# Optimization experiments

Hardware: AMD Instinct MI355X
Metric: run time of the kernel (lower is better)

## Reference

```python
import jax, jax.numpy as jnp
import numpy as np

B = 8192
E = 8
H = 128
NUM_CLASSES = 3
SIM_THRESHOLD = 0.8
EFF_THRESHOLD = 0.1
TARGET_TEMP = 1.0
W_LB, W_EFF, W_CONS, W_ENT, W_TEMP = 0.1, 0.05, 0.1, 0.01, 0.01


def setup_inputs() -> dict:
    key = jax.random.key(0)
    k1, k2, k3, k4 = jax.random.split(key, 4)
    logits = jax.random.normal(k1, (B, NUM_CLASSES), dtype=jnp.float32)
    targets = jax.random.randint(k2, (B,), 0, NUM_CLASSES, dtype=jnp.int64)
    raw = jax.random.uniform(k3, (B, E), dtype=jnp.float32)
    routing_probs = raw / raw.sum(axis=-1, keepdims=True)  # rows sum to 1
    input_embeddings = jax.random.uniform(k4, (B, H), dtype=jnp.float32)
    temperature = jnp.ones((1,), dtype=jnp.float32)
    return {
        "logits": logits,
        "targets": targets,
        "routing_probs": routing_probs,
        "input_embeddings": input_embeddings,
        "temperature": temperature,
    }


def _dynamo_loss(logits, routing_probs, input_embeddings, temperature, targets):
    # --- task loss: cross entropy (sentiment) ---
    logp_cls = jax.nn.log_softmax(logits, axis=-1)
    task_loss = -jnp.take_along_axis(logp_cls, targets[:, None], axis=-1).mean()

    # --- load balance: var(mean usage) / (1/E)^2 (torch.var unbiased) ---
    expert_usage = routing_probs.mean(axis=0)  # [E]
    lb_loss = W_LB * jnp.var(expert_usage, ddof=1) * (E ** 2)

    # --- efficiency: sum of probs below threshold, averaged over batch ---
    small = jnp.where(routing_probs < EFF_THRESHOLD, routing_probs, 0.0)
    eff_loss = W_EFF * small.sum(axis=-1).mean()

    # --- consistency: masked pairwise KL over similar samples ---
    nrm = input_embeddings / jnp.linalg.norm(input_embeddings, axis=-1, keepdims=True)
    sim = nrm @ nrm.T  # [B, B]
    mask = (sim > SIM_THRESHOLD) & ~jnp.eye(B, dtype=bool)
    logp = jax.nn.log_softmax(routing_probs, axis=-1)  # [B, E]
    p = jnp.exp(logp)
    a = jnp.sum(p * logp, axis=-1)  # [B], sum_e p_j log p_j
    # KL(i,j) = sum_e p_j (log p_j - log p_i) = a[j] - logp[i] . p[j]
    kl = a[None, :] - logp @ p.T  # [B, B]
    num_pairs = mask.sum()
    kl_sum = jnp.sum(jnp.where(mask, kl, 0.0))
    cons_loss = W_CONS * jnp.where(num_pairs > 0, kl_sum / jnp.maximum(num_pairs, 1), 0.0)

    # --- entropy regularization (maximize entropy of routing_probs-as-probs) ---
    eps = 1e-8
    entropy = -jnp.sum(routing_probs * jnp.log(routing_probs + eps), axis=-1)
    ent_loss = W_ENT * (-entropy.mean())

    # --- temperature regularization ---
    temp_loss = W_TEMP * jnp.mean((temperature - TARGET_TEMP) ** 2)

    return task_loss + lb_loss + eff_loss + cons_loss + ent_loss + temp_loss


def reference(logits, targets, routing_probs, input_embeddings, temperature):
    return _dynamo_loss(logits, routing_probs, input_embeddings, temperature, targets)
```

## Files before the change

### kernel.cpp

```cpp
#include <hip/hip_runtime.h>
#include <stdint.h>

#define B_SZ 8192
#define LOG8 2.0794415416798357f
#define NTILE 2080

typedef __attribute__((ext_vector_type(8))) short short8;
typedef __attribute__((ext_vector_type(4))) float floatx4;

__device__ inline unsigned short f2bf(float f) {
    unsigned int u = __float_as_uint(f);
    u = (u + 0x7FFFu + ((u >> 16) & 1u)) >> 16;
    return (unsigned short)u;
}
__device__ inline float bf2f(unsigned short s) {
    return __uint_as_float(((unsigned int)s) << 16);
}
__device__ inline float wredf(float x) {
#pragma unroll
    for (int o = 32; o; o >>= 1) x += __shfl_down(x, o);
    return x;
}
__device__ inline int wredi(int x) {
#pragma unroll
    for (int o = 32; o; o >>= 1) x += __shfl_down(x, o);
    return x;
}


__global__ __launch_bounds__(512) void prep_all(
    const float* __restrict__ logits,
    const int* __restrict__ targets,
    const float* __restrict__ routing,
    const float* __restrict__ emb,
    unsigned short* __restrict__ nrm,
    unsigned short* __restrict__ nlq,
    unsigned short* __restrict__ pb,
    float* __restrict__ aprime,
    float* __restrict__ prepslot) {
    __shared__ float pred[8][11];
    const int bid = blockIdx.x;
    const int lane = threadIdx.x & 63;
    const int wave = threadIdx.x >> 6;

    if (bid < 256) {
#pragma unroll
        for (int iter = 0; iter < 4; ++iter) {
            int row = (((iter << 8) + bid) << 3) + wave;
            const float2* e2 = (const float2*)(emb + (size_t)row * 128);
            float2 v = e2[lane];
            float ss = v.x * v.x + v.y * v.y;
            ss = wredf(ss);
            ss = __shfl(ss, 0);
            float inv = rsqrtf(ss);
            ushort2 o;
            o.x = f2bf(v.x * inv);
            o.y = f2bf(v.y * inv);
            ((ushort2*)(nrm + (size_t)row * 128))[lane] = o;
        }
        return;
    }

    int row = ((bid - 256) << 9) + threadIdx.x;

    const float4* r4 = (const float4*)(routing + (size_t)row * 8);
    float4 va = r4[0], vb = r4[1];
    float v[8] = {va.x, va.y, va.z, va.w, vb.x, vb.y, vb.z, vb.w};

    float mx = v[0];
#pragma unroll
    for (int e = 1; e < 8; ++e) mx = fmaxf(mx, v[e]);
    float ex[8], s = 0.f;
#pragma unroll
    for (int e = 0; e < 8; ++e) { ex[e] = expf(v[e] - mx); s += ex[e]; }
    float ls = logf(s);
    float inv_s = 1.f / s;

    union { unsigned short u[8]; uint4 q; } lu, pu;
    float ap = 0.f;
#pragma unroll
    for (int e = 0; e < 8; ++e) {
        unsigned short pe = f2bf(ex[e] * inv_s);
        unsigned short le = f2bf(v[e] - mx - ls + LOG8);
        pu.u[e] = pe;
        lu.u[e] = le ^ 0x8000;
        ap += bf2f(pe) * bf2f(le);
    }
    ((uint4*)nlq)[row] = lu.q;
    ((uint4*)pb)[row] = pu.q;
    aprime[row] = ap;

    float eff = 0.f, ent = 0.f;
#pragma unroll
    for (int e = 0; e < 8; ++e) {
        if (v[e] < 0.1f) eff += v[e];
        ent += v[e] * logf(v[e] + 1e-8f);
    }

    const float* lg = logits + (size_t)row * 3;
    float a0 = lg[0], a1 = lg[1], a2 = lg[2];
    float mm = fmaxf(a0, fmaxf(a1, a2));
    float lse = mm + logf(expf(a0 - mm) + expf(a1 - mm) + expf(a2 - mm));
    int tg = targets[row];
    float tv = (tg == 0) ? a0 : ((tg == 1) ? a1 : a2);
    float task = lse - tv;

    task = wredf(task);
    eff = wredf(eff);
    ent = wredf(ent);
    float cs[8];
#pragma unroll
    for (int e = 0; e < 8; ++e) cs[e] = wredf(v[e]);

    if (lane == 0) {
        pred[wave][0] = task;
        pred[wave][1] = eff;
        pred[wave][2] = ent;
#pragma unroll
        for (int e = 0; e < 8; ++e) pred[wave][3 + e] = cs[e];
    }
    __syncthreads();
    if (threadIdx.x < 11) {
        float s2 = 0.f;
#pragma unroll
        for (int w = 0; w < 8; ++w) s2 += pred[w][threadIdx.x];
        prepslot[(bid - 256) * 11 + threadIdx.x] = s2;
    }
}

__global__ __launch_bounds__(512, 4) void tile_sym(
    const unsigned short* __restrict__ nrm,
    const unsigned short* __restrict__ nlq,
    const unsigned short* __restrict__ pb,
    const float* __restrict__ aprime,
    float* __restrict__ klslot,
    unsigned int* __restrict__ cntslot) {
    __shared__ uint4 sh[2][128][16];

    const int t = threadIdx.x;
    const int L = blockIdx.x;

    int bi = (int)((129.0f - sqrtf((float)(16641 - 8 * L))) * 0.5f);
    int T = bi * 64 - ((bi * (bi - 1)) >> 1);
    while (L < T) { --bi; T = bi * 64 - ((bi * (bi - 1)) >> 1); }
    while (L >= T + (64 - bi)) { T += 64 - bi; ++bi; }
    const int bj = bi + (L - T);
    const bool diag = (bi == bj);
    const int iBase = bi << 7, jBase = bj << 7;

    const uint4* n4 = (const uint4*)nrm;
#pragma unroll
    for (int it = 0; it < 4; ++it) {
        int c = t + (it << 9);
        int row = c >> 4, g = c & 15;
        int gp = g ^ (row & 15);
        uint4 va = n4[((size_t)(iBase + row) << 4) + g];
        uint4 vb = n4[((size_t)(jBase + row) << 4) + g];
        sh[0][row][gp] = va;
        sh[1][row][gp] = vb;
    }

    const int wave = t >> 6, lane = t & 63;
    const int wr = wave >> 2, wc = wave & 3;
    const int m = lane & 15, q = lane >> 4;
    const short8 zero8 = (short8){0, 0, 0, 0, 0, 0, 0, 0};

    short8 crA[4], crB[2];
#pragma unroll
    for (int a = 0; a < 4; ++a) {
        int ri = iBase + (wr << 6) + (a << 4) + m;
        short8 v = zero8;
        if (q == 0) v = *(const short8*)&nlq[(size_t)ri << 3];
        else if (q == 1) { if (!diag) v = *(const short8*)&pb[(size_t)ri << 3]; }
        else if (q == 2) {
            v[1] = (short)0x3F80;
            if (!diag) v[0] = (short)f2bf(aprime[ri]);
        }
        crA[a] = v;
    }
#pragma unroll
    for (int b = 0; b < 2; ++b) {
        int cj = jBase + (wc << 5) + (b << 4) + m;
        short8 v = zero8;
        if (q == 0) v = *(const short8*)&pb[(size_t)cj << 3];
        else if (q == 1) v = *(const short8*)&nlq[(size_t)cj << 3];
        else if (q == 2) {
            v[0] = (short)0x3F80;
            v[1] = (short)f2bf(aprime[cj]);
        }
        crB[b] = v;
    }

    __syncthreads();

    const unsigned short* Ab = (const unsigned short*)&sh[0][0][0];
    const unsigned short* Bb = (const unsigned short*)&sh[1][0][0];

    floatx4 simacc[4][2];
#pragma unroll
    for (int a = 0; a < 4; ++a)
#pragma unroll
        for (int b = 0; b < 2; ++b) simacc[a][b] = (floatx4){0.f, 0.f, 0.f, 0.f};

#pragma unroll
    for (int ks = 0; ks < 4; ++ks) {
        const int g = (ks << 2) + q;
        short8 af[4], bfr[2];
#pragma unroll
        for (int a = 0; a < 4; ++a) {
            int ra = (wr << 6) + (a << 4) + m;
            af[a] = *(const short8*)&Ab[(ra << 7) + ((g ^ m) << 3)];
        }
#pragma unroll
        for (int b = 0; b < 2; ++b) {
            int rb = (wc << 5) + (b << 4) + m;
            bfr[b] = *(const short8*)&Bb[(rb << 7) + ((g ^ m) << 3)];
        }
#pragma unroll
        for (int a = 0; a < 4; ++a)
#pragma unroll
            for (int b = 0; b < 2; ++b)
                simacc[a][b] = __builtin_amdgcn_mfma_f32_16x16x32_bf16(
                    af[a], bfr[b], simacc[a][b], 0, 0, 0);
    }

    float klLocal = 0.f;
    int cntLocal = 0;
#pragma unroll
    for (int a = 0; a < 4; ++a) {
        const int gRow0 = iBase + (wr << 6) + (a << 4) + (q << 2);
#pragma unroll
        for (int b = 0; b < 2; ++b) {
            const int gCol = jBase + (wc << 5) + (b << 4) + m;
            floatx4 cr = __builtin_amdgcn_mfma_f32_16x16x32_bf16(
                crA[a], crB[b], (floatx4){0.f, 0.f, 0.f, 0.f}, 0, 0, 0);
            if (diag) {
#pragma unroll
                for (int r = 0; r < 4; ++r) {
                    if ((simacc[a][b][r] > 0.8f) && (gRow0 + r != gCol)) {
                        klLocal += cr[r];
                        cntLocal += 1;
                    }
                }
            } else {
#pragma unroll
                for (int r = 0; r < 4; ++r) {
                    if (simacc[a][b][r] > 0.8f) {
                        klLocal += cr[r];
                        cntLocal += 2;
                    }
                }
            }
        }
    }

    klLocal = wredf(klLocal);
    cntLocal = wredi(cntLocal);

    __syncthreads();
    float* redk = (float*)&sh[0][0][0];
    int* redc = (int*)(redk + 8);
    if (lane == 0) { redk[wave] = klLocal; redc[wave] = cntLocal; }
    __syncthreads();

    if (t == 0) {
        float k = 0.f;
        int c = 0;
#pragma unroll
        for (int w = 0; w < 8; ++w) { k += redk[w]; c += redc[w]; }
        klslot[L] = k;
        cntslot[L] = (unsigned int)c;
    }
}

__global__ void finalize_k(const float* __restrict__ klslot,
                           const unsigned int* __restrict__ cntslot,
                           const float* __restrict__ prepslot,
                           const float* __restrict__ temp,
                           float* __restrict__ out) {
    __shared__ float sk[4];
    __shared__ int sc[4];
    __shared__ float sp[11];
    const int t = threadIdx.x, lane = t & 63, wave = t >> 6;

    float k = 0.f;
    int c = 0;
    for (int i = t; i < NTILE; i += 256) { k += klslot[i]; c += (int)cntslot[i]; }
    k = wredf(k);
    c = wredi(c);
    if (lane == 0) { sk[wave] = k; sc[wave] = c; }
    if (t < 11) {
        float s = 0.f;
        for (int r = 0; r < 16; ++r) s += prepslot[r * 11 + t];
        sp[t] = s;
    }
    __syncthreads();
    if (t == 0) {
        float K = sk[0] + sk[1] + sk[2] + sk[3];
        int C = sc[0] + sc[1] + sc[2] + sc[3];
        const float invB = 1.f / (float)B_SZ;
        float task = sp[0] * invB;
        float eff = 0.05f * sp[1] * invB;
        float entl = 0.01f * sp[2] * invB;
        float cons = 0.1f * (C > 0 ? K / (float)C : 0.f);
        float u[8], mean = 0.f;
        for (int e = 0; e < 8; ++e) { u[e] = sp[3 + e] * invB; mean += u[e]; }
        mean *= 0.125f;
        float var = 0.f;
        for (int e = 0; e < 8; ++e) { float d = u[e] - mean; var += d * d; }
        var *= (1.f / 7.f);
        float lb = 0.1f * var * 64.f;
        float tt = temp[0] - 1.f;
        out[0] = task + lb + eff + cons + entl + 0.01f * tt * tt;
    }
}

extern "C" void kernel_launch(void* const* d_in, const int* in_sizes, int n_in,
                              void* d_out, int out_size, void* d_ws, size_t ws_size,
                              hipStream_t stream) {
    const float* logits = (const float*)d_in[0];
    const int* targets = (const int*)d_in[1];
    const float* routing = (const float*)d_in[2];
    const float* emb = (const float*)d_in[3];
    const float* temp = (const float*)d_in[4];

    char* ws = (char*)d_ws;
    unsigned short* nrm = (unsigned short*)ws;
    unsigned short* nlq = (unsigned short*)(ws + 2097152);
    unsigned short* pb = (unsigned short*)(ws + 2228224);
    float* aprime = (float*)(ws + 2359296);
    float* klslot = (float*)(ws + 2392064);
    unsigned int* cntslot = (unsigned int*)(ws + 2400384);
    float* prepslot = (float*)(ws + 2408704);

    prep_all<<<272, 512, 0, stream>>>(logits, targets, routing, emb,
                                      nrm, nlq, pb, aprime, prepslot);
    tile_sym<<<NTILE, 512, 0, stream>>>(nrm, nlq, pb, aprime, klslot, cntslot);
    finalize_k<<<1, 256, 0, stream>>>(klslot, cntslot, prepslot, temp,
                                      (float*)d_out);
}
```

Before: 103.2 us.

## Load embedding tiles via async global_load_lds in two K-halves

Replaces register-staged global-to-LDS copies of the normalized-embedding tiles with direct global_load_lds async copies, split into two K halves. The first half's MFMAs run while the second half is still loading, and the LDS layout changes to a per-half 8-slot XOR swizzle. The aim is to cut VGPR staging and overlap load latency with compute. It relies on correct synchronization of the async LDS writes: __syncthreads may not wait on vmcnt for these loads, which could cause races.

```diff
diff --git a/kernel.cpp b/kernel.cpp
--- a/kernel.cpp
+++ b/kernel.cpp
@@ -7,6 +7,13 @@
 
 typedef __attribute__((ext_vector_type(8))) short short8;
 typedef __attribute__((ext_vector_type(4))) float floatx4;
+
+typedef __attribute__((address_space(1))) const uint4 guint4;
+typedef __attribute__((address_space(3))) uint4 luint4;
+
+__device__ inline void async_cp16(const uint4* g, uint4* l) {
+    __builtin_amdgcn_global_load_lds((guint4*)g, (luint4*)l, 16, 0, 0);
+}
 
 __device__ inline unsigned short f2bf(float f) {
     unsigned int u = __float_as_uint(f);
@@ -135,10 +142,11 @@
     const float* __restrict__ aprime,
     float* __restrict__ klslot,
     unsigned int* __restrict__ cntslot) {
-    __shared__ uint4 sh[2][128][16];
+    __shared__ uint4 sh[4096];
 
     const int t = threadIdx.x;
     const int L = blockIdx.x;
+    const int wave = t >> 6, lane = t & 63;
 
     int bi = (int)((129.0f - sqrtf((float)(16641 - 8 * L))) * 0.5f);
     int T = bi * 64 - ((bi * (bi - 1)) >> 1);
@@ -149,18 +157,22 @@
     const int iBase = bi << 7, jBase = bj << 7;
 
     const uint4* n4 = (const uint4*)nrm;
-#pragma unroll
-    for (int it = 0; it < 4; ++it) {
-        int c = t + (it << 9);
-        int row = c >> 4, g = c & 15;
-        int gp = g ^ (row & 15);
-        uint4 va = n4[((size_t)(iBase + row) << 4) + g];
-        uint4 vb = n4[((size_t)(jBase + row) << 4) + g];
-        sh[0][row][gp] = va;
-        sh[1][row][gp] = vb;
-    }
-
-    const int wave = t >> 6, lane = t & 63;
+    const int s0 = t & 7, r0 = t >> 3;
+    const int s1 = (t + 512) & 7, r1 = (t + 512) >> 3;
+    const int g0 = s0 ^ (r0 & 7), g1 = s1 ^ (r1 & 7);
+
+    async_cp16(&n4[((size_t)(iBase + r0) << 4) + g0], sh + (wave << 6));
+    async_cp16(&n4[((size_t)(iBase + r1) << 4) + g1], sh + 512 + (wave << 6));
+    async_cp16(&n4[((size_t)(jBase + r0) << 4) + g0], sh + 1024 + (wave << 6));
+    async_cp16(&n4[((size_t)(jBase + r1) << 4) + g1], sh + 1536 + (wave << 6));
+
+    __syncthreads();
+
+    async_cp16(&n4[((size_t)(iBase + r0) << 4) + 8 + g0], sh + 2048 + (wave << 6));
+    async_cp16(&n4[((size_t)(iBase + r1) << 4) + 8 + g1], sh + 2560 + (wave << 6));
+    async_cp16(&n4[((size_t)(jBase + r0) << 4) + 8 + g0], sh + 3072 + (wave << 6));
+    async_cp16(&n4[((size_t)(jBase + r1) << 4) + 8 + g1], sh + 3584 + (wave << 6));
+
     const int wr = wave >> 2, wc = wave & 3;
     const int m = lane & 15, q = lane >> 4;
     const short8 zero8 = (short8){0, 0, 0, 0, 0, 0, 0, 0};
@@ -191,31 +203,46 @@
         crB[b] = v;
     }
 
-    __syncthreads();
-
-    const unsigned short* Ab = (const unsigned short*)&sh[0][0][0];
-    const unsigned short* Bb = (const unsigned short*)&sh[1][0][0];
-
     floatx4 simacc[4][2];
 #pragma unroll
     for (int a = 0; a < 4; ++a)
 #pragma unroll
         for (int b = 0; b < 2; ++b) simacc[a][b] = (floatx4){0.f, 0.f, 0.f, 0.f};
 
-#pragma unroll
-    for (int ks = 0; ks < 4; ++ks) {
-        const int g = (ks << 2) + q;
+    const int m7 = m & 7;
+    const int raOff = (wr << 6) << 3;
+    const int rbOff = (wc << 5) << 3;
+
+#pragma unroll
+    for (int ks = 0; ks < 2; ++ks) {
+        const int sg = ((ks << 2) + q) ^ m7;
         short8 af[4], bfr[2];
 #pragma unroll
-        for (int a = 0; a < 4; ++a) {
-            int ra = (wr << 6) + (a << 4) + m;
-            af[a] = *(const short8*)&Ab[(ra << 7) + ((g ^ m) << 3)];
-        }
-#pragma unroll
-        for (int b = 0; b < 2; ++b) {
-            int rb = (wc << 5) + (b << 4) + m;
-            bfr[b] = *(const short8*)&Bb[(rb << 7) + ((g ^ m) << 3)];
-        }
+        for (int a = 0; a < 4; ++a)
+            af[a] = *(const short8*)(sh + raOff + (((a << 4) + m) << 3) + sg);
+#pragma unroll
+        for (int b = 0; b < 2; ++b)
+            bfr[b] = *(const short8*)(sh + 1024 + rbOff + (((b << 4) + m) << 3) + sg);
+#pragma unroll
+        for (int a = 0; a < 4; ++a)
+#pragma unroll
+            for (int b = 0; b < 2; ++b)
+                simacc[a][b] = __builtin_amdgcn_mfma_f32_16x16x32_bf16(
+                    af[a], bfr[b], simacc[a][b], 0, 0, 0);
+    }
+
+    __syncthreads();
+
+#pragma unroll
+    for (int ks = 0; ks < 2; ++ks) {
+        const int sg = ((ks << 2) + q) ^ m7;
+        short8 af[4], bfr[2];
+#pragma unroll
+        for (int a = 0; a < 4; ++a)
+            af[a] = *(const short8*)(sh + 2048 + raOff + (((a << 4) + m) << 3) + sg);
+#pragma unroll
+        for (int b = 0; b < 2; ++b)
+            bfr[b] = *(const short8*)(sh + 3072 + rbOff + (((b << 4) + m) << 3) + sg);
 #pragma unroll
         for (int a = 0; a < 4; ++a)
 #pragma unroll
@@ -258,7 +285,7 @@
     cntLocal = wredi(cntLocal);
 
     __syncthreads();
-    float* redk = (float*)&sh[0][0][0];
+    float* redk = (float*)sh;
     int* redc = (int*)(redk + 8);
     if (lane == 0) { redk[wave] = klLocal; redc[wave] = cntLocal; }
     __syncthreads();
```

Measured after the change: 101.9 us. No clear change (-1.2%).

## Stage A tile via async global-to-LDS loads and read B fragments directly

Applied to the files above, without the earlier changes.

The A-side embedding tile is now copied into shared memory with the hardware's direct global-to-LDS load path instead of going through registers. The B-side fragments are loaded straight from global memory into registers, which halves LDS usage and drops the B-side LDS reads. The similarity MFMA loop now runs before the routing fragment setup. This is meant to cut register staging and LDS traffic and to allow more concurrent blocks, at the cost of uncoalesced-ish direct global fragment loads and reliance on the async LDS copy's layout semantics (the wave-based LDS destination must match the swizzled read indexing).

```diff
diff --git a/kernel.cpp b/kernel.cpp
--- a/kernel.cpp
+++ b/kernel.cpp
@@ -7,6 +7,13 @@
 
 typedef __attribute__((ext_vector_type(8))) short short8;
 typedef __attribute__((ext_vector_type(4))) float floatx4;
+
+typedef __attribute__((address_space(1))) const uint4 guint4;
+typedef __attribute__((address_space(3))) uint4 luint4;
+
+__device__ inline void async_cp16(const uint4* g, uint4* l) {
+    __builtin_amdgcn_global_load_lds((guint4*)g, (luint4*)l, 16, 0, 0);
+}
 
 __device__ inline unsigned short f2bf(float f) {
     unsigned int u = __float_as_uint(f);
@@ -135,10 +142,11 @@
     const float* __restrict__ aprime,
     float* __restrict__ klslot,
     unsigned int* __restrict__ cntslot) {
-    __shared__ uint4 sh[2][128][16];
+    __shared__ uint4 sh[2048];
 
     const int t = threadIdx.x;
     const int L = blockIdx.x;
+    const int wave = t >> 6, lane = t & 63;
 
     int bi = (int)((129.0f - sqrtf((float)(16641 - 8 * L))) * 0.5f);
     int T = bi * 64 - ((bi * (bi - 1)) >> 1);
@@ -149,22 +157,54 @@
     const int iBase = bi << 7, jBase = bj << 7;
 
     const uint4* n4 = (const uint4*)nrm;
+
 #pragma unroll
     for (int it = 0; it < 4; ++it) {
-        int c = t + (it << 9);
-        int row = c >> 4, g = c & 15;
-        int gp = g ^ (row & 15);
-        uint4 va = n4[((size_t)(iBase + row) << 4) + g];
-        uint4 vb = n4[((size_t)(jBase + row) << 4) + g];
-        sh[0][row][gp] = va;
-        sh[1][row][gp] = vb;
-    }
-
-    const int wave = t >> 6, lane = t & 63;
+        int idx = t + (it << 9);
+        int row = idx >> 4, s = idx & 15;
+        int g = s ^ (row & 15);
+        async_cp16(&n4[((size_t)(iBase + row) << 4) + g],
+                   sh + (it << 9) + (wave << 6));
+    }
+
     const int wr = wave >> 2, wc = wave & 3;
     const int m = lane & 15, q = lane >> 4;
+
+    const int colB0 = jBase + (wc << 5) + m;
+    short8 bfr[4][2];
+#pragma unroll
+    for (int ks = 0; ks < 4; ++ks)
+#pragma unroll
+        for (int b = 0; b < 2; ++b)
+            bfr[ks][b] = *(const short8*)&nrm[(size_t)(colB0 + (b << 4)) * 128 +
+                                              (ks << 5) + (q << 3)];
+
+    __syncthreads();
+
+    floatx4 simacc[4][2];
+#pragma unroll
+    for (int a = 0; a < 4; ++a)
+#pragma unroll
+        for (int b = 0; b < 2; ++b) simacc[a][b] = (floatx4){0.f, 0.f, 0.f, 0.f};
+
+#pragma unroll
+    for (int ks = 0; ks < 4; ++ks) {
+        const int gk = (ks << 2) + q;
+        short8 af[4];
+#pragma unroll
+        for (int a = 0; a < 4; ++a) {
+            int row = (wr << 6) + (a << 4) + m;
+            af[a] = *(const short8*)(sh + (row << 4) + (gk ^ m));
+        }
+#pragma unroll
+        for (int a = 0; a < 4; ++a)
+#pragma unroll
+            for (int b = 0; b < 2; ++b)
+                simacc[a][b] = __builtin_amdgcn_mfma_f32_16x16x32_bf16(
+                    af[a], bfr[ks][b], simacc[a][b], 0, 0, 0);
+    }
+
     const short8 zero8 = (short8){0, 0, 0, 0, 0, 0, 0, 0};
-
     short8 crA[4], crB[2];
 #pragma unroll
     for (int a = 0; a < 4; ++a) {
@@ -191,39 +231,6 @@
         crB[b] = v;
     }
 
-    __syncthreads();
-
-    const unsigned short* Ab = (const unsigned short*)&sh[0][0][0];
-    const unsigned short* Bb = (const unsigned short*)&sh[1][0][0];
-
-    floatx4 simacc[4][2];
-#pragma unroll
-    for (int a = 0; a < 4; ++a)
-#pragma unroll
-        for (int b = 0; b < 2; ++b) simacc[a][b] = (floatx4){0.f, 0.f, 0.f, 0.f};
-
-#pragma unroll
-    for (int ks = 0; ks < 4; ++ks) {
-        const int g = (ks << 2) + q;
-        short8 af[4], bfr[2];
-#pragma unroll
-        for (int a = 0; a < 4; ++a) {
-            int ra = (wr << 6) + (a << 4) + m;
-            af[a] = *(const short8*)&Ab[(ra << 7) + ((g ^ m) << 3)];
-        }
-#pragma unroll
-        for (int b = 0; b < 2; ++b) {
-            int rb = (wc << 5) + (b << 4) + m;
-            bfr[b] = *(const short8*)&Bb[(rb << 7) + ((g ^ m) << 3)];
-        }
-#pragma unroll
-        for (int a = 0; a < 4; ++a)
-#pragma unroll
-            for (int b = 0; b < 2; ++b)
-                simacc[a][b] = __builtin_amdgcn_mfma_f32_16x16x32_bf16(
-                    af[a], bfr[b], simacc[a][b], 0, 0, 0);
-    }
-
     float klLocal = 0.f;
     int cntLocal = 0;
 #pragma unroll
@@ -258,7 +265,7 @@
     cntLocal = wredi(cntLocal);
 
     __syncthreads();
-    float* redk = (float*)&sh[0][0][0];
+    float* redk = (float*)sh;
     int* redc = (int*)(redk + 8);
     if (lane == 0) { redk[wave] = klLocal; redc[wave] = cntLocal; }
     __syncthreads();
```

New measurement: 107.2 us. 1.04x slower.
